# Performance work log

Measured on AMD Instinct MI355X. Metric: run time of the kernel, lower is better.

## Reference

```python
import jax, jax.numpy as jnp
from jax import lax
import numpy as np


def setup_inputs() -> dict:
    key = jax.random.key(0)
    ks = iter(jax.random.split(key, 48))

    def w(shape):
        fan = shape[0] if len(shape) == 2 else int(np.prod(shape[1:]))
        return jax.random.normal(next(ks), shape, jnp.float32) / np.sqrt(fan)

    def b(n):
        return jax.random.normal(next(ks), (n,), jnp.float32) * 0.01

    T = 16
    return dict(
        search=jax.random.normal(next(ks), (3, 383, 287), jnp.float32),
        exemplars=jax.random.normal(next(ks), (T, 3, 383, 287), jnp.float32),
        # AlexNet features (random-weight stand-in for pretrained)
        aw1=w((64, 3, 11, 11)), ab1=b(64),
        aw2=w((192, 64, 5, 5)), ab2=b(192),
        aw3=w((384, 192, 3, 3)), ab3=b(384),
        aw4=w((256, 384, 3, 3)), ab4=b(256),
        aw5=w((256, 256, 3, 3)), ab5=b(256),
        # conv_deconv: Conv1d(256,256,3,p=1) -> MaxPool1d(88) -> ConvTranspose1d(256,256,88)
        wcd=w((256, 256, 3)), bcd=b(256),
        wt=w((256, 256, 88)), bt=b(256),
        # st_gcn: GCN(256, 512, 256)
        ws1=w((256, 512)), bs1=b(512),
        ws2=w((512, 256)), bs2=b(256),
        # g, h: 1x1 Conv1d(256,256) == linear maps
        wg=w((256, 256)), bg=b(256),
        wh=w((256, 256)), bh=b(256),
        # ct_gcn: GCN(256, 384, 256)
        wc1=w((256, 384)), bc1=b(384),
        wc2=w((384, 256)), bc2=b(256),
    )


def _gct_forward(search, exemplars, aw1, ab1, aw2, ab2, aw3, ab3, aw4, ab4,
                 aw5, ab5, wcd, bcd, wt, bt, ws1, bs1, ws2, bs2,
                 wg, bg, wh, bh, wc1, bc1, wc2, bc2):
    f32 = jnp.float32

    def conv2d(x, w, bias, s, p):
        y = lax.conv_general_dilated(x, w, (s, s), [(p, p), (p, p)],
                                     dimension_numbers=('NCHW', 'OIHW', 'NCHW'))
        return y + bias[None, :, None, None]

    def maxpool(x):  # k=3, s=2, VALID (AlexNet pools)
        return lax.reduce_window(x, -jnp.inf, lax.max, (1, 1, 3, 3), (1, 1, 2, 2), 'VALID')

    def features(x):
        x = maxpool(jax.nn.relu(conv2d(x, aw1, ab1, 4, 2)))
        x = maxpool(jax.nn.relu(conv2d(x, aw2, ab2, 1, 2)))
        x = jax.nn.relu(conv2d(x, aw3, ab3, 1, 1))
        x = jax.nn.relu(conv2d(x, aw4, ab4, 1, 1))
        x = maxpool(jax.nn.relu(conv2d(x, aw5, ab5, 1, 1)))
        return x

    lrelu = lambda v: jax.nn.leaky_relu(v, 0.01)

    X = features(search[None])          # [1,256,11,8]
    Z = features(exemplars)             # [T,256,11,8]
    T = Z.shape[0]
    D = X.shape[1]                      # 256
    M = X.shape[2] * X.shape[3]         # 88
    Xf = X.reshape(D, M)                # [256,88]
    Zf = Z.reshape(T, D, M)             # [T,256,88]

    # conv_deconv branch: conv1d(k=3,p=1) -> global maxpool -> conv_transpose(k=M)
    xc = lax.conv_general_dilated(Xf[None], wcd, (1,), [(1, 1)],
                                  dimension_numbers=('NCH', 'OIH', 'NCH'))[0] + bcd[:, None]
    v = jnp.max(xc, axis=1)                              # [256]
    X_hat = jnp.einsum('i,iok->ok', v, wt) + bt[:, None]  # [256,88]

    # spatiotemporal graph: A[i+T*j, i+T*k]=1 for j!=k; self-loops for t!=0
    TM = T * M
    n = jnp.arange(TM)
    same_t = (n[:, None] % T) == (n[None, :] % T)
    diff_s = (n[:, None] // T) != (n[None, :] // T)
    A1 = (same_t & diff_s).astype(f32) + jnp.diag((n % T != 0).astype(f32))

    # st GCN over TM nodes (node n = t + T*m -> spatial-major flatten)
    nodes = Zf.transpose(2, 0, 1).reshape(TM, D)          # [TM,256]
    h1 = lrelu(A1 @ (nodes @ ws1) + bs1)                  # [TM,512]
    h2 = lrelu(A1 @ (h1 @ ws2) + bs2)                     # [TM,256]
    V1 = jnp.max(h2.reshape(M, T, D), axis=1).T           # temporal max-pool -> [256,88]

    # dynamic cross-track graph: pairwise g/h affinities + row softmax (fused)
    Vx = V1 + X_hat                                       # [256,88]
    G = wg @ Vx + bg[:, None]                             # [256,88]
    Hh = wh @ Vx + bh[:, None]                            # [256,88]
    A2 = jax.nn.softmax(Hh.T @ G, axis=1)                 # [88,88], A2[j,i]=g(i).h(j)

    # ct GCN
    xv = V1.T                                             # [88,256]
    c1 = lrelu(A2 @ (xv @ wc1) + bc1)                     # [88,384]
    V2 = lrelu(A2 @ (c1 @ wc2) + bc2).T                   # [256,88]

    # F.conv2d(X[1,256,11,8], V2[1,256,11,8]) -> full-overlap correlation = scalar
    R = jnp.sum(Xf * V2).reshape(1, 1, 1, 1)
    return R


def reference(search, exemplars, aw1, ab1, aw2, ab2, aw3, ab3, aw4, ab4,
              aw5, ab5, wcd, bcd, wt, bt, ws1, bs1, ws2, bs2,
              wg, bg, wh, bh, wc1, bc1, wc2, bc2):
    return _gct_forward(search, exemplars, aw1, ab1, aw2, ab2, aw3, ab3, aw4, ab4,
                        aw5, ab5, wcd, bcd, wt, bt, ws1, bs1, ws2, bs2,
                        wg, bg, wh, bh, wc1, bc1, wc2, bc2)
```

## Files before the change

### kernel.cpp

```cpp
#include <hip/hip_runtime.h>
#include <hip/hip_bf16.h>
#include <math.h>

#define BATCH 17
#define T_EX 16
#define H0 383
#define W0 287
#define C1 64
#define H1 95
#define W1 71
#define H1P 47
#define W1P 35
#define C2 192
#define H2P 23
#define W2P 17
#define C3 384
#define C45 256
#define H5P 11
#define W5P 8
#define DD 256
#define MM 88
#define TM 1408

#define HP1 389
#define WP1 292

typedef unsigned short ushort_t;
typedef __attribute__((ext_vector_type(8))) short short8;
typedef __attribute__((ext_vector_type(4))) float f32x4;

__device__ __forceinline__ float lrelu(float v) { return v > 0.f ? v : 0.01f * v; }

__device__ __forceinline__ ushort_t f2bf(float f) {
    unsigned int u = __float_as_uint(f);
    unsigned int r = (u + 0x7fffu + ((u >> 16) & 1u)) >> 16;
    return (ushort_t)r;
}
__device__ __forceinline__ float b2f(ushort_t b) {
    return __uint_as_float(((unsigned int)b) << 16);
}
__device__ __forceinline__ short8 ld16(const ushort_t* p) { return *(const short8*)p; }
__device__ __forceinline__ short8 ld2x8(const ushort_t* p) {
    union { uint2 u[2]; short8 s; } uu;
    uu.u[0] = *(const uint2*)p;
    uu.u[1] = *(const uint2*)(p + 4);
    return uu.s;
}
__device__ __forceinline__ void async_cp16(ushort_t* l, const ushort_t* g) {
    __builtin_amdgcn_global_load_lds(
        (const __attribute__((address_space(1))) void*)g,
        (__attribute__((address_space(3))) void*)l, 16, 0, 0);
}

__global__ void zfill_k(float4* __restrict__ p, int n4) {
    int idx = blockIdx.x * 256 + threadIdx.x;
    if (idx < n4) p[idx] = (float4){0.f, 0.f, 0.f, 0.f};
}

__global__ void prep1_k(const float* __restrict__ search, const float* __restrict__ exemp,
                        ushort_t* __restrict__ out) {
    int idx = blockIdx.x * 256 + threadIdx.x;
    if (idx >= BATCH * H0 * W0) return;
    int ix = idx % W0; int t = idx / W0;
    int iy = t % H0; int b = t / H0;
    const float* src = (b == 0) ? search : exemp + (size_t)(b - 1) * 3 * H0 * W0;
    const int hw = H0 * W0;
    float v0 = src[iy * W0 + ix];
    float v1 = src[hw + iy * W0 + ix];
    float v2 = src[2 * hw + iy * W0 + ix];
    ushort4 o;
    o.x = f2bf(v0); o.y = f2bf(v1); o.z = f2bf(v2); o.w = 0;
    *(ushort4*)&out[(((size_t)b * HP1 + iy + 2) * WP1 + ix + 2) * 4] = o;
}

__global__ void wprep_k(const float* __restrict__ w, ushort_t* __restrict__ out,
                        int KH, int KWl, int KWr, int CINl, int CINr,
                        int NKS, int nch) {
    int idx = blockIdx.x * 256 + threadIdx.x;
    if (idx >= nch) return;
    int c = idx & 255;
    int rest = idx >> 8;
    int ks = rest % NKS;
    int ocb = rest / NKS;
    int k8 = c >> 6, m = c & 63;
    int oc = ocb * 64 + m;
    int KWC = KWl * CINl;
    ushort_t* o = out + (size_t)idx * 8;
#pragma unroll
    for (int j = 0; j < 8; ++j) {
        int kg = ks * 32 + k8 * 8 + j;
        int ky = kg / KWC; int rem = kg - ky * KWC;
        int kx = rem / CINl; int ic = rem - kx * CINl;
        float v = 0.f;
        if (ky < KH && kx < KWr && ic < CINr)
            v = w[(((size_t)oc * CINr + ic) * KH + ky) * KWr + kx];
        o[j] = f2bf(v);
    }
}

__global__ void wprep_gemm_k(const float* __restrict__ ws1, const float* __restrict__ ws2,
                             const float* __restrict__ wcd, ushort_t* __restrict__ WS1T,
                             ushort_t* __restrict__ WS2T, ushort_t* __restrict__ WCDT) {
    int idx = blockIdx.x * 256 + threadIdx.x;
    const float* src; ushort_t* dst; int NKS, mode = 0, sa = 1, sk = 0, base;
    if (idx < 16384)       { src = ws1; dst = WS1T; NKS = 8;  sk = 512; base = idx; }
    else if (idx < 32768)  { src = ws2; dst = WS2T; NKS = 16; sk = 256; base = idx - 16384; }
    else if (idx < 57344)  { src = wcd; dst = WCDT; NKS = 24; mode = 1; base = idx - 32768; }
    else return;
    int c = base & 255;
    int rest = base >> 8;
    int ks = rest % NKS;
    int ocb = rest / NKS;
    int k8 = c >> 6, m = c & 63;
    int oc = ocb * 64 + m;
    ushort_t* o = dst + (size_t)base * 8;
#pragma unroll
    for (int j = 0; j < 8; ++j) {
        int kg = ks * 32 + k8 * 8 + j;
        float v;
        if (mode == 0) v = src[(size_t)oc * sa + (size_t)kg * sk];
        else           v = src[(size_t)oc * 768 + (kg & 255) * 3 + (kg >> 8)];
        o[j] = f2bf(v);
    }
}

template <int STRIDE, bool A16>
__global__ __launch_bounds__(256) void conv_mfma5(
    const ushort_t* __restrict__ inp, const ushort_t* __restrict__ wt,
    const float* __restrict__ bias, ushort_t* __restrict__ out,
    int Hp, int Wp, int C, int Wout, int HW, int NKS2, int KWl,
    int OHp, int OWp, int OPAD, int COUT) {
    const int tid = threadIdx.x;
    const int wv = tid >> 6, lane = tid & 63;
    const int quad = lane >> 4, l16 = lane & 15;
    const int n_blk = blockIdx.x * 64;
    const int ocb = blockIdx.y;
    const int b = blockIdx.z;

    __shared__ ushort_t As[2][4096];
    __shared__ ushort_t Bs[2][4096];
    __shared__ int offs[432];

    const int KWC = KWl * C;
    for (int g = tid; g < NKS2 * 8; g += 256) {
        int kg = g * 8;
        int ky = kg / KWC; int rem = kg - ky * KWC;
        int kx = rem / C; int c8 = rem - kx * C;
        offs[g] = (ky * Wp + kx) * C + c8;
    }

    const ushort_t* inb = inp + (size_t)b * Hp * Wp * C;
    int n_g = n_blk + lane;
    int n_gc = n_g < HW ? n_g : HW - 1;
    int oy = n_gc / Wout, ox = n_gc - oy * Wout;
    const int base0 = (oy * STRIDE * Wp + ox * STRIDE) * C;

    f32x4 acc[4];
#pragma unroll
    for (int cn = 0; cn < 4; ++cn) acc[cn] = (f32x4){0.f, 0.f, 0.f, 0.f};

    const ushort_t* wblk = wt + (size_t)ocb * (size_t)NKS2 * 4096;

    __syncthreads();

    {
        const ushort_t* aS = wblk + tid * 8;
        async_cp16(&As[0][tid * 8], aS);
        async_cp16(&As[0][2048 + tid * 8], aS + 2048);
        const int o0 = offs[wv], o1 = offs[4 + wv];
        if (A16) {
            async_cp16(&Bs[0][tid * 8], inb + base0 + o0);
            async_cp16(&Bs[0][2048 + tid * 8], inb + base0 + o1);
        } else {
            *(short8*)&Bs[0][tid * 8] = ld2x8(inb + base0 + o0);
            *(short8*)&Bs[0][2048 + tid * 8] = ld2x8(inb + base0 + o1);
        }
    }
    __syncthreads();

    for (int ks2 = 0; ks2 < NKS2; ++ks2) {
        const int cur = ks2 & 1, nxt = cur ^ 1;
        if (ks2 + 1 < NKS2) {
            const ushort_t* aS = wblk + (size_t)(ks2 + 1) * 4096 + tid * 8;
            async_cp16(&As[nxt][tid * 8], aS);
            async_cp16(&As[nxt][2048 + tid * 8], aS + 2048);
            const int o0 = offs[(ks2 + 1) * 8 + wv], o1 = offs[(ks2 + 1) * 8 + 4 + wv];
            if (A16) {
                async_cp16(&Bs[nxt][tid * 8], inb + base0 + o0);
                async_cp16(&Bs[nxt][2048 + tid * 8], inb + base0 + o1);
            } else {
                *(short8*)&Bs[nxt][tid * 8] = ld2x8(inb + base0 + o0);
                *(short8*)&Bs[nxt][2048 + tid * 8] = ld2x8(inb + base0 + o1);
            }
        }
#pragma unroll
        for (int h = 0; h < 2; ++h) {
            const short8 af = *(const short8*)&As[cur][h * 2048 + (quad * 64 + wv * 16 + l16) * 8];
#pragma unroll
            for (int cn = 0; cn < 4; ++cn) {
                const short8 bfr = *(const short8*)&Bs[cur][h * 2048 + (quad * 64 + cn * 16 + l16) * 8];
                acc[cn] = __builtin_amdgcn_mfma_f32_16x16x32_bf16(af, bfr, acc[cn], 0, 0, 0);
            }
        }
        __syncthreads();
    }

    const int oc0 = ocb * 64 + wv * 16 + quad * 4;
    const float bi0 = bias[oc0], bi1 = bias[oc0 + 1], bi2 = bias[oc0 + 2], bi3 = bias[oc0 + 3];
#pragma unroll
    for (int cn = 0; cn < 4; ++cn) {
        int n = n_blk + cn * 16 + l16;
        if (n < HW) {
            int y = n / Wout, x = n - y * Wout;
            size_t base = (((size_t)b * OHp + y + OPAD) * OWp + x + OPAD) * COUT + oc0;
            ushort4 o;
            o.x = f2bf(fmaxf(acc[cn][0] + bi0, 0.f));
            o.y = f2bf(fmaxf(acc[cn][1] + bi1, 0.f));
            o.z = f2bf(fmaxf(acc[cn][2] + bi2, 0.f));
            o.w = f2bf(fmaxf(acc[cn][3] + bi3, 0.f));
            *(ushort4*)&out[base] = o;
        }
    }
}

template <int MODE, bool HASBIAS, bool SC1>
__global__ __launch_bounds__(256) void gemm_mfma3(
    const ushort_t* __restrict__ Bsrc, const ushort_t* __restrict__ wt,
    const float* __restrict__ bias, float* __restrict__ out,
    int RS, int N, int NKS, int sn, int sc) {
    const int tid = threadIdx.x;
    const int wv = tid >> 6, lane = tid & 63;
    const int quad = lane >> 4, l16 = lane & 15;
    const int n_blk = blockIdx.x * 64;
    const int ocb = blockIdx.y;

    __shared__ ushort_t Bs[2][2048];

    int n_g = n_blk + lane;
    int n_gc = n_g < N ? n_g : N - 1;
    int row = (MODE == 1) ? (1 + (n_gc & 15)) * MM + (n_gc >> 4) : n_gc;
    const size_t base0 = (size_t)row * RS;

    f32x4 acc[4];
#pragma unroll
    for (int cn = 0; cn < 4; ++cn) acc[cn] = (f32x4){0.f, 0.f, 0.f, 0.f};

    const ushort_t* wblk = wt + (size_t)ocb * NKS * 2048;
    const int afrag = (quad * 64 + wv * 16 + l16) * 8;

    short8 a0 = ld16(wblk + afrag);
    *(short8*)&Bs[0][tid * 8] = ld16(Bsrc + base0 + wv * 8);
    __syncthreads();

    for (int ks = 0; ks < NKS; ++ks) {
        const int cur = ks & 1, nxt = cur ^ 1;
        short8 a1, bn;
        const bool more = (ks + 1 < NKS);
        if (more) {
            a1 = ld16(wblk + (ks + 1) * 2048 + afrag);
            bn = ld16(Bsrc + base0 + (ks + 1) * 32 + wv * 8);
        }
#pragma unroll
        for (int cn = 0; cn < 4; ++cn) {
            const short8 bfr = *(const short8*)&Bs[cur][(quad * 64 + cn * 16 + l16) * 8];
            acc[cn] = __builtin_amdgcn_mfma_f32_16x16x32_bf16(a0, bfr, acc[cn], 0, 0, 0);
        }
        if (more) *(short8*)&Bs[nxt][tid * 8] = bn;
        a0 = a1;
        __syncthreads();
    }

    const int oc0 = ocb * 64 + wv * 16 + quad * 4;
    float bb[4] = {0.f, 0.f, 0.f, 0.f};
    if (HASBIAS) { bb[0] = bias[oc0]; bb[1] = bias[oc0+1]; bb[2] = bias[oc0+2]; bb[3] = bias[oc0+3]; }
#pragma unroll
    for (int cn = 0; cn < 4; ++cn) {
        int n = n_blk + cn * 16 + l16;
        if (n < N) {
            if (SC1) {
                float4 o;
                o.x = acc[cn][0] + bb[0]; o.y = acc[cn][1] + bb[1];
                o.z = acc[cn][2] + bb[2]; o.w = acc[cn][3] + bb[3];
                *(float4*)&out[(size_t)n * sn + oc0] = o;
            } else {
#pragma unroll
                for (int reg = 0; reg < 4; ++reg)
                    out[(size_t)n * sn + (size_t)(oc0 + reg) * sc] = acc[cn][reg] + bb[reg];
            }
        }
    }
}

__global__ void pool_nhwc(const ushort_t* __restrict__ in, ushort_t* __restrict__ out,
                          int C, int Hin, int Win, int Hout, int Wout,
                          int OHp, int OWp, int OPAD) {
    int total = BATCH * C * Hout * Wout;
    int idx = blockIdx.x * 256 + threadIdx.x;
    if (idx >= total) return;
    int c = idx % C; int r = idx / C;
    int x = r % Wout; r /= Wout;
    int y = r % Hout; int b = r / Hout;
    const int rs = Win * C;
    const ushort_t* p = in + (((size_t)b * Hin + 2 * y) * Win + 2 * x) * C + c;
    float m = b2f(p[0]);
    m = fmaxf(m, b2f(p[C])); m = fmaxf(m, b2f(p[2 * C]));
    m = fmaxf(m, b2f(p[rs])); m = fmaxf(m, b2f(p[rs + C])); m = fmaxf(m, b2f(p[rs + 2 * C]));
    m = fmaxf(m, b2f(p[2 * rs])); m = fmaxf(m, b2f(p[2 * rs + C])); m = fmaxf(m, b2f(p[2 * rs + 2 * C]));
    out[(((size_t)b * OHp + y + OPAD) * OWp + x + OPAD) * C + c] = f2bf(m);
}

__global__ void pool5_k(const ushort_t* __restrict__ in, float* __restrict__ P,
                        ushort_t* __restrict__ PB, ushort_t* __restrict__ XfPad) {
    int total = BATCH * 256 * MM;
    int idx = blockIdx.x * 256 + threadIdx.x;
    if (idx >= total) return;
    int c = idx % 256; int r = idx / 256;
    int x = r % W5P; r /= W5P;
    int y = r % H5P; int b = r / H5P;
    const int rs = W2P * 256;
    const ushort_t* p = in + (((size_t)b * H2P + 2 * y) * W2P + 2 * x) * 256 + c;
    float m = b2f(p[0]);
    m = fmaxf(m, b2f(p[256])); m = fmaxf(m, b2f(p[512]));
    m = fmaxf(m, b2f(p[rs])); m = fmaxf(m, b2f(p[rs + 256])); m = fmaxf(m, b2f(p[rs + 512]));
    m = fmaxf(m, b2f(p[2 * rs])); m = fmaxf(m, b2f(p[2 * rs + 256])); m = fmaxf(m, b2f(p[2 * rs + 512]));
    int mm = y * W5P + x;
    size_t o = ((size_t)b * MM + mm) * 256 + c;
    P[o] = m;
    ushort_t mb = f2bf(m);
    PB[o] = mb;
    if (b == 0) XfPad[(size_t)(mm + 1) * 256 + c] = mb;
}

__global__ void vmax_k(const float* __restrict__ xc, float* __restrict__ v) {
    int c = blockIdx.x * 64 + threadIdx.x;
    float m = -INFINITY;
    for (int j = 0; j < MM; ++j) m = fmaxf(m, xc[(size_t)c * MM + j]);
    v[c] = m;
}

__global__ void xhat_k(const float* __restrict__ v, const float* __restrict__ wt,
                       const float* __restrict__ bt, float* __restrict__ xhat) {
    __shared__ float lv[256];
    for (int j = threadIdx.x; j < 256; j += 256) lv[j] = v[j];
    __syncthreads();
    int idx = blockIdx.x * 256 + threadIdx.x;
    if (idx >= DD * MM) return;
    int k = idx % MM, o = idx / MM;
    float acc = bt[o];
    for (int i = 0; i < 256; ++i) acc = fmaf(lv[i], wt[(i * 256 + o) * MM + k], acc);
    xhat[idx] = acc;
}

__global__ void s1_k(const float* __restrict__ Y1, float* __restrict__ S1) {
    int idx = blockIdx.x * 256 + threadIdx.x;
    if (idx >= T_EX * 512) return;
    int c = idx % 512, t = idx / 512;
    float acc = 0.f;
    for (int m = 0; m < MM; ++m) acc += Y1[(m * T_EX + t) * 512 + c];
    S1[idx] = acc;
}

__global__ void h1_k(const float* __restrict__ Y1, const float* __restrict__ S1,
                     const float* __restrict__ bs1, ushort_t* __restrict__ h1b) {
    int idx = blockIdx.x * 256 + threadIdx.x;
    if (idx >= TM * 512) return;
    int c = idx % 512; int n = idx / 512;
    int t = n % T_EX;
    float val = S1[t * 512 + c] + bs1[c];
    if (t == 0) val -= Y1[idx];
    h1b[idx] = f2bf(lrelu(val));
}

__global__ void s2_k(const float* __restrict__ Y2, float* __restrict__ S2) {
    int idx = blockIdx.x * 256 + threadIdx.x;
    if (idx >= T_EX * 256) return;
    int c = idx % 256, t = idx / 256;
    float acc = 0.f;
    for (int m = 0; m < MM; ++m) acc += Y2[(m * T_EX + t) * 256 + c];
    S2[idx] = acc;
}

__global__ void h2_k(const float* __restrict__ Y2, const float* __restrict__ S2,
                     const float* __restrict__ bs2, float* __restrict__ h2) {
    int idx = blockIdx.x * 256 + threadIdx.x;
    if (idx >= TM * 256) return;
    int c = idx % 256; int n = idx / 256;
    int t = n % T_EX;
    float val = S2[t * 256 + c] + bs2[c];
    if (t == 0) val -= Y2[idx];
    h2[idx] = lrelu(val);
}

__global__ void v1vx_k(const float* __restrict__ h2, const float* __restrict__ xhat,
                       float* __restrict__ V1, float* __restrict__ Vx) {
    int idx = blockIdx.x * 256 + threadIdx.x;
    if (idx >= DD * MM) return;
    int m = idx % MM, d = idx / MM;
    float mx = -INFINITY;
    for (int t = 0; t < T_EX; ++t) mx = fmaxf(mx, h2[(m * T_EX + t) * 256 + d]);
    V1[idx] = mx;
    Vx[idx] = mx + xhat[idx];
}

__global__ void lin88_k(const float* __restrict__ Wg, const float* __restrict__ bg,
                        const float* __restrict__ Wh, const float* __restrict__ bh,
                        const float* __restrict__ Vin, float* __restrict__ Gout,
                        float* __restrict__ Hout) {
    int idx = blockIdx.x * 256 + threadIdx.x;
    if (idx >= DD * MM) return;
    const float* W = blockIdx.y ? Wh : Wg;
    const float* bias = blockIdx.y ? bh : bg;
    float* out = blockIdx.y ? Hout : Gout;
    int m = idx % MM, o = idx / MM;
    const float* wr = W + o * 256;
    float acc = bias[o];
    for (int i = 0; i < 256; ++i) acc = fmaf(wr[i], Vin[i * MM + m], acc);
    out[idx] = acc;
}

__global__ void smsm_k(const float* __restrict__ Hh, const float* __restrict__ G,
                       float* __restrict__ A2) {
    int j = blockIdx.x;
    int tid = threadIdx.x;
    __shared__ float row[96];
    __shared__ float red[128];
    for (int i = tid; i < MM; i += 128) {
        float acc = 0.f;
        for (int c = 0; c < 256; ++c) acc = fmaf(Hh[c * MM + j], G[c * MM + i], acc);
        row[i] = acc;
    }
    __syncthreads();
    float val = (tid < MM) ? row[tid] : -INFINITY;
    red[tid] = val; __syncthreads();
    for (int s = 64; s > 0; s >>= 1) {
        if (tid < s) red[tid] = fmaxf(red[tid], red[tid + s]);
        __syncthreads();
    }
    float mx = red[0]; __syncthreads();
    float e = (tid < MM) ? expf(val - mx) : 0.f;
    red[tid] = e; __syncthreads();
    for (int s = 64; s > 0; s >>= 1) {
        if (tid < s) red[tid] += red[tid + s];
        __syncthreads();
    }
    float inv = 1.f / red[0];
    if (tid < MM) A2[j * MM + tid] = e * inv;
}

__global__ void t1_k(const float* __restrict__ V1, const float* __restrict__ wc1,
                     float* __restrict__ t1) {
    int idx = blockIdx.x * 256 + threadIdx.x;
    if (idx >= MM * 384) return;
    int c = idx % 384, m = idx / 384;
    float acc = 0.f;
    for (int d = 0; d < 256; ++d) acc = fmaf(V1[d * MM + m], wc1[d * 384 + c], acc);
    t1[idx] = acc;
}

__global__ void c1_k(const float* __restrict__ A2, const float* __restrict__ t1,
                     const float* __restrict__ bc1, float* __restrict__ c1) {
    int idx = blockIdx.x * 256 + threadIdx.x;
    if (idx >= MM * 384) return;
    int c = idx % 384, j = idx / 384;
    float acc = bc1[c];
    for (int i = 0; i < MM; ++i) acc = fmaf(A2[j * MM + i], t1[i * 384 + c], acc);
    c1[idx] = lrelu(acc);
}

__global__ void t2_k(const float* __restrict__ c1, const float* __restrict__ wc2,
                     float* __restrict__ t2) {
    int idx = blockIdx.x * 256 + threadIdx.x;
    if (idx >= MM * 256) return;
    int c = idx % 256, m = idx / 256;
    const float* cr = c1 + m * 384;
    float acc = 0.f;
    for (int d = 0; d < 384; ++d) acc = fmaf(cr[d], wc2[d * 256 + c], acc);
    t2[idx] = acc;
}

__global__ void v2_k(const float* __restrict__ A2, const float* __restrict__ t2,
                     const float* __restrict__ bc2, float* __restrict__ V2m) {
    int idx = blockIdx.x * 256 + threadIdx.x;
    if (idx >= MM * 256) return;
    int c = idx % 256, j = idx / 256;
    float acc = bc2[c];
    for (int i = 0; i < MM; ++i) acc = fmaf(A2[j * MM + i], t2[i * 256 + c], acc);
    V2m[idx] = lrelu(acc);
}

__global__ void final_k(const float* __restrict__ Xf2, const float* __restrict__ V2m,
                        float* __restrict__ out) {
    __shared__ float red[256];
    float acc = 0.f;
    for (int idx = threadIdx.x; idx < DD * MM; idx += 256)
        acc = fmaf(Xf2[idx], V2m[idx], acc);
    red[threadIdx.x] = acc; __syncthreads();
    for (int s = 128; s > 0; s >>= 1) {
        if (threadIdx.x < s) red[threadIdx.x] += red[threadIdx.x + s];
        __syncthreads();
    }
    if (threadIdx.x == 0) out[0] = red[0];
}

extern "C" void kernel_launch(void* const* d_in, const int* in_sizes, int n_in,
                              void* d_out, int out_size, void* d_ws, size_t ws_size,
                              hipStream_t stream) {
    const float* search = (const float*)d_in[0];
    const float* exemp  = (const float*)d_in[1];
    const float* aw1 = (const float*)d_in[2];  const float* ab1 = (const float*)d_in[3];
    const float* aw2 = (const float*)d_in[4];  const float* ab2 = (const float*)d_in[5];
    const float* aw3 = (const float*)d_in[6];  const float* ab3 = (const float*)d_in[7];
    const float* aw4 = (const float*)d_in[8];  const float* ab4 = (const float*)d_in[9];
    const float* aw5 = (const float*)d_in[10]; const float* ab5 = (const float*)d_in[11];
    const float* wcd = (const float*)d_in[12]; const float* bcd = (const float*)d_in[13];
    const float* wt  = (const float*)d_in[14]; const float* bt  = (const float*)d_in[15];
    const float* ws1 = (const float*)d_in[16]; const float* bs1 = (const float*)d_in[17];
    const float* ws2 = (const float*)d_in[18]; const float* bs2 = (const float*)d_in[19];
    const float* wg  = (const float*)d_in[20]; const float* bg  = (const float*)d_in[21];
    const float* wh  = (const float*)d_in[22]; const float* bh  = (const float*)d_in[23];
    const float* wc1 = (const float*)d_in[24]; const float* bc1 = (const float*)d_in[25];
    const float* wc2 = (const float*)d_in[26]; const float* bc2 = (const float*)d_in[27];

    float* ws = (float*)d_ws;
    float* R1 = ws;
    float* R2 = ws + 3870720;
    float* R3 = ws + 7544832;
    float* Wg = ws + 8628864;

    ushort_t* in1p  = (ushort_t*)R1;
    ushort_t* c1out = (ushort_t*)R2;
    ushort_t* p1out = (ushort_t*)R3;
    ushort_t* c2out = (ushort_t*)R1;
    ushort_t* p2out = (ushort_t*)R2;
    ushort_t* c3out = (ushort_t*)(R2 + 775200);
    ushort_t* c4out = (ushort_t*)R1;
    ushort_t* c5out = (ushort_t*)R3;
    ushort_t* WT    = (ushort_t*)Wg;

    zfill_k<<<(965500 + 255) / 256, 256, 0, stream>>>((float4*)R1, 965500);
    prep1_k<<<(BATCH * H0 * W0 + 255) / 256, 256, 0, stream>>>(search, exemp, in1p);
    wprep_k<<<(4608 + 255) / 256, 256, 0, stream>>>(aw1, WT, 11, 12, 11, 4, 3, 18, 4608);
    conv_mfma5<4, false><<<dim3(106, 1, BATCH), 256, 0, stream>>>(
        in1p, WT, ab1, c1out, HP1, WP1, 4, W1, H1 * W1, 9, 12, H1, W1, 0, 64);
    zfill_k<<<(270504 + 255) / 256, 256, 0, stream>>>((float4*)R3, 270504);
    pool_nhwc<<<(BATCH * 64 * H1P * W1P + 255) / 256, 256, 0, stream>>>(
        c1out, p1out, 64, H1, W1, H1P, W1P, 51, 39, 2);
    wprep_k<<<(38400 + 255) / 256, 256, 0, stream>>>(aw2, WT, 5, 5, 5, 64, 64, 50, 38400);
    conv_mfma5<1, true><<<dim3(26, 3, BATCH), 256, 0, stream>>>(
        p1out, WT, ab2, c2out, 51, 39, 64, W1P, H1P * W1P, 25, 5, H1P, W1P, 0, 192);
    zfill_k<<<(581400 + 255) / 256, 256, 0, stream>>>((float4*)R2, 581400);
    pool_nhwc<<<(BATCH * 192 * H2P * W2P + 255) / 256, 256, 0, stream>>>(
        c2out, p2out, 192, H1P, W1P, H2P, W2P, 25, 19, 1);
    wprep_k<<<(82944 + 255) / 256, 256, 0, stream>>>(aw3, WT, 3, 3, 3, 192, 192, 54, 82944);
    conv_mfma5<1, true><<<dim3(7, 6, BATCH), 256, 0, stream>>>(
        p2out, WT, ab3, c3out, 25, 19, 192, W2P, H2P * W2P, 27, 3, 25, 19, 1, 384);
    zfill_k<<<(258400 + 255) / 256, 256, 0, stream>>>((float4*)R1, 258400);
    wprep_k<<<(110592 + 255) / 256, 256, 0, stream>>>(aw4, WT, 3, 3, 3, 384, 384, 108, 110592);
    conv_mfma5<1, true><<<dim3(7, 4, BATCH), 256, 0, stream>>>(
        c3out, WT, ab4, c4out, 25, 19, 384, W2P, H2P * W2P, 54, 3, 25, 19, 1, 256);
    wprep_k<<<(73728 + 255) / 256, 256, 0, stream>>>(aw5, WT, 3, 3, 3, 256, 256, 72, 73728);
    conv_mfma5<1, true><<<dim3(7, 4, BATCH), 256, 0, stream>>>(
        c4out, WT, ab5, c5out, 25, 19, 256, W2P, H2P * W2P, 36, 3, H2P, W2P, 0, 256);

    float*    P      = R1 + 2417664;
    ushort_t* PB     = (ushort_t*)(R1 + 2800640);
    ushort_t* XfPad  = (ushort_t*)(R1 + 2992128);
    float*    xc     = R1 + 3003648;

    ushort_t* WS1T = (ushort_t*)Wg;
    ushort_t* WS2T = (ushort_t*)(Wg + 65536);
    ushort_t* WCDT = (ushort_t*)(Wg + 131072);
    wprep_gemm_k<<<(57344 + 255) / 256, 256, 0, stream>>>(ws1, ws2, wcd, WS1T, WS2T, WCDT);

    pool5_k<<<(BATCH * 256 * MM + 255) / 256, 256, 0, stream>>>(c5out, P, PB, XfPad);
    float* Xf2 = P;

    float* v_   = R1 + 0;
    float* xhat = R1 + 1024;
    float* Y1   = R1 + 23552;
    float* S1   = R1 + 744448;
    ushort_t* h1b = (ushort_t*)(R1 + 752640);
    float* Y2   = R1 + 1473536;
    float* S2   = R1 + 1833984;
    float* h2   = R1 + 1838080;
    float* V1   = R1 + 2198528;
    float* Vx   = R1 + 2221056;
    float* G    = R1 + 2243584;
    float* Hh   = R1 + 2266112;
    float* A2   = R1 + 2296832;
    float* t1   = R1 + 2305024;
    float* c1   = R1 + 2338816;
    float* t2   = R1 + 2372608;
    float* V2m  = R1 + 2395136;

    gemm_mfma3<0, true, false><<<dim3(2, 4), 256, 0, stream>>>(
        XfPad, WCDT, bcd, xc, 256, MM, 24, 1, MM);
    vmax_k<<<4, 64, 0, stream>>>(xc, v_);
    xhat_k<<<(DD * MM + 255) / 256, 256, 0, stream>>>(v_, wt, bt, xhat);

    gemm_mfma3<1, false, true><<<dim3(22, 8), 256, 0, stream>>>(
        PB, WS1T, nullptr, Y1, 256, TM, 8, 512, 1);
    s1_k<<<(T_EX * 512 + 255) / 256, 256, 0, stream>>>(Y1, S1);
    h1_k<<<(TM * 512 + 255) / 256, 256, 0, stream>>>(Y1, S1, bs1, h1b);
    gemm_mfma3<0, false, true><<<dim3(22, 4), 256, 0, stream>>>(
        h1b, WS2T, nullptr, Y2, 512, TM, 16, 256, 1);
    s2_k<<<(T_EX * 256 + 255) / 256, 256, 0, stream>>>(Y2, S2);
    h2_k<<<(TM * 256 + 255) / 256, 256, 0, stream>>>(Y2, S2, bs2, h2);
    v1vx_k<<<(DD * MM + 255) / 256, 256, 0, stream>>>(h2, xhat, V1, Vx);

    lin88_k<<<dim3((DD * MM + 255) / 256, 2), 256, 0, stream>>>(wg, bg, wh, bh, Vx, G, Hh);
    smsm_k<<<MM, 128, 0, stream>>>(Hh, G, A2);

    t1_k<<<(MM * 384 + 255) / 256, 256, 0, stream>>>(V1, wc1, t1);
    c1_k<<<(MM * 384 + 255) / 256, 256, 0, stream>>>(A2, t1, bc1, c1);
    t2_k<<<(MM * 256 + 255) / 256, 256, 0, stream>>>(c1, wc2, t2);
    v2_k<<<(MM * 256 + 255) / 256, 256, 0, stream>>>(A2, t2, bc2, V2m);

    final_k<<<1, 256, 0, stream>>>(Xf2, V2m, (float*)d_out);
}
```

Baseline: 547.6 us.

## Register-stage conv B tiles with XOR-swizzled LDS and fuse small epilogue kernels

The conv kernel's B-operand (activation) loads for the A16 path now go through registers and are written into a swizzled LDS layout after the MFMA loop, instead of direct async copies. Each 8-lane group fetches one pixel's contiguous channels, and the XOR swizzle is meant to reduce LDS bank conflicts on the fragment reads. Separately, the vmax+xhat kernels and the s1/h1 and s2/h2 reduction/broadcast pairs are each fused into a single kernel to cut launches and intermediate buffers. wprep_k also gains an output-channel bound guard. The register staging trades async overlap for coalescing and conflict-free reads, and the fused kernels run far fewer threads per pass.

```diff
diff --git a/kernel.cpp b/kernel.cpp
--- a/kernel.cpp
+++ b/kernel.cpp
@@ -75,7 +75,7 @@
 
 __global__ void wprep_k(const float* __restrict__ w, ushort_t* __restrict__ out,
                         int KH, int KWl, int KWr, int CINl, int CINr,
-                        int NKS, int nch) {
+                        int NKS, int nch, int OCr) {
     int idx = blockIdx.x * 256 + threadIdx.x;
     if (idx >= nch) return;
     int c = idx & 255;
@@ -92,7 +92,7 @@
         int ky = kg / KWC; int rem = kg - ky * KWC;
         int kx = rem / CINl; int ic = rem - kx * CINl;
         float v = 0.f;
-        if (ky < KH && kx < KWr && ic < CINr)
+        if (oc < OCr && ky < KH && kx < KWr && ic < CINr)
             v = w[(((size_t)oc * CINr + ic) * KH + ky) * KWr + kx];
         o[j] = f2bf(v);
     }
@@ -125,7 +125,7 @@
 }
 
 template <int STRIDE, bool A16>
-__global__ __launch_bounds__(256) void conv_mfma5(
+__global__ __launch_bounds__(256) void conv_mfma13(
     const ushort_t* __restrict__ inp, const ushort_t* __restrict__ wt,
     const float* __restrict__ bias, ushort_t* __restrict__ out,
     int Hp, int Wp, int C, int Wout, int HW, int NKS2, int KWl,
@@ -150,10 +150,25 @@
     }
 
     const ushort_t* inb = inp + (size_t)b * Hp * Wp * C;
+
+    const int g8 = lane & 7, po = lane >> 3;
+    int np0 = n_blk + wv * 16 + po;      if (np0 >= HW) np0 = HW - 1;
+    int np1 = n_blk + wv * 16 + 8 + po;  if (np1 >= HW) np1 = HW - 1;
+    const ushort_t* bsrc0;
+    const ushort_t* bsrc1;
+    {
+        int oy0 = np0 / Wout, ox0 = np0 - oy0 * Wout;
+        int oy1 = np1 / Wout, ox1 = np1 - oy1 * Wout;
+        bsrc0 = inb + (size_t)(oy0 * STRIDE * Wp + ox0 * STRIDE) * C;
+        bsrc1 = inb + (size_t)(oy1 * STRIDE * Wp + ox1 * STRIDE) * C;
+    }
+    const int ws0 = g8 * 512 + (((wv * 16 + po) ^ g8) * 8);
+    const int ws1 = g8 * 512 + (((wv * 16 + 8 + po) ^ g8) * 8);
+
     int n_g = n_blk + lane;
     int n_gc = n_g < HW ? n_g : HW - 1;
-    int oy = n_gc / Wout, ox = n_gc - oy * Wout;
-    const int base0 = (oy * STRIDE * Wp + ox * STRIDE) * C;
+    int oyl = n_gc / Wout, oxl = n_gc - oyl * Wout;
+    const int base0 = (oyl * STRIDE * Wp + oxl * STRIDE) * C;
 
     f32x4 acc[4];
 #pragma unroll
@@ -167,11 +182,13 @@
         const ushort_t* aS = wblk + tid * 8;
         async_cp16(&As[0][tid * 8], aS);
         async_cp16(&As[0][2048 + tid * 8], aS + 2048);
-        const int o0 = offs[wv], o1 = offs[4 + wv];
-        if (A16) {
-            async_cp16(&Bs[0][tid * 8], inb + base0 + o0);
-            async_cp16(&Bs[0][2048 + tid * 8], inb + base0 + o1);
+        if constexpr (A16) {
+            short8 r0v = ld16(bsrc0 + offs[g8]);
+            short8 r1v = ld16(bsrc1 + offs[g8]);
+            *(short8*)&Bs[0][ws0] = r0v;
+            *(short8*)&Bs[0][ws1] = r1v;
         } else {
+            const int o0 = offs[wv], o1 = offs[4 + wv];
             *(short8*)&Bs[0][tid * 8] = ld2x8(inb + base0 + o0);
             *(short8*)&Bs[0][2048 + tid * 8] = ld2x8(inb + base0 + o1);
         }
@@ -180,15 +197,17 @@
 
     for (int ks2 = 0; ks2 < NKS2; ++ks2) {
         const int cur = ks2 & 1, nxt = cur ^ 1;
-        if (ks2 + 1 < NKS2) {
+        const bool more = (ks2 + 1 < NKS2);
+        short8 rb0, rb1;
+        if (more) {
             const ushort_t* aS = wblk + (size_t)(ks2 + 1) * 4096 + tid * 8;
             async_cp16(&As[nxt][tid * 8], aS);
             async_cp16(&As[nxt][2048 + tid * 8], aS + 2048);
-            const int o0 = offs[(ks2 + 1) * 8 + wv], o1 = offs[(ks2 + 1) * 8 + 4 + wv];
-            if (A16) {
-                async_cp16(&Bs[nxt][tid * 8], inb + base0 + o0);
-                async_cp16(&Bs[nxt][2048 + tid * 8], inb + base0 + o1);
+            if constexpr (A16) {
+                rb0 = ld16(bsrc0 + offs[(ks2 + 1) * 8 + g8]);
+                rb1 = ld16(bsrc1 + offs[(ks2 + 1) * 8 + g8]);
             } else {
+                const int o0 = offs[(ks2 + 1) * 8 + wv], o1 = offs[(ks2 + 1) * 8 + 4 + wv];
                 *(short8*)&Bs[nxt][tid * 8] = ld2x8(inb + base0 + o0);
                 *(short8*)&Bs[nxt][2048 + tid * 8] = ld2x8(inb + base0 + o1);
             }
@@ -198,8 +217,19 @@
             const short8 af = *(const short8*)&As[cur][h * 2048 + (quad * 64 + wv * 16 + l16) * 8];
 #pragma unroll
             for (int cn = 0; cn < 4; ++cn) {
-                const short8 bfr = *(const short8*)&Bs[cur][h * 2048 + (quad * 64 + cn * 16 + l16) * 8];
+                int bidx;
+                if constexpr (A16)
+                    bidx = h * 2048 + quad * 512 + (((cn * 16 + l16) ^ (h * 4 + quad)) * 8);
+                else
+                    bidx = h * 2048 + (quad * 64 + cn * 16 + l16) * 8;
+                const short8 bfr = *(const short8*)&Bs[cur][bidx];
                 acc[cn] = __builtin_amdgcn_mfma_f32_16x16x32_bf16(af, bfr, acc[cn], 0, 0, 0);
+            }
+        }
+        if constexpr (A16) {
+            if (more) {
+                *(short8*)&Bs[nxt][ws0] = rb0;
+                *(short8*)&Bs[nxt][ws1] = rb1;
             }
         }
         __syncthreads();
@@ -331,17 +361,16 @@
     if (b == 0) XfPad[(size_t)(mm + 1) * 256 + c] = mb;
 }
 
-__global__ void vmax_k(const float* __restrict__ xc, float* __restrict__ v) {
-    int c = blockIdx.x * 64 + threadIdx.x;
-    float m = -INFINITY;
-    for (int j = 0; j < MM; ++j) m = fmaxf(m, xc[(size_t)c * MM + j]);
-    v[c] = m;
-}
-
-__global__ void xhat_k(const float* __restrict__ v, const float* __restrict__ wt,
-                       const float* __restrict__ bt, float* __restrict__ xhat) {
+__global__ void xhat2_k(const float* __restrict__ xc, const float* __restrict__ wt,
+                        const float* __restrict__ bt, float* __restrict__ xhat) {
     __shared__ float lv[256];
-    for (int j = threadIdx.x; j < 256; j += 256) lv[j] = v[j];
+    {
+        int j = threadIdx.x;
+        const float* xr = xc + (size_t)j * MM;
+        float mx = xr[0];
+        for (int k = 1; k < MM; ++k) mx = fmaxf(mx, xr[k]);
+        lv[j] = mx;
+    }
     __syncthreads();
     int idx = blockIdx.x * 256 + threadIdx.x;
     if (idx >= DD * MM) return;
@@ -351,44 +380,41 @@
     xhat[idx] = acc;
 }
 
-__global__ void s1_k(const float* __restrict__ Y1, float* __restrict__ S1) {
+__global__ void sh1_k(const float* __restrict__ Y1, const float* __restrict__ bs1,
+                      ushort_t* __restrict__ h1b) {
     int idx = blockIdx.x * 256 + threadIdx.x;
     if (idx >= T_EX * 512) return;
-    int c = idx % 512, t = idx / 512;
-    float acc = 0.f;
-    for (int m = 0; m < MM; ++m) acc += Y1[(m * T_EX + t) * 512 + c];
-    S1[idx] = acc;
-}
-
-__global__ void h1_k(const float* __restrict__ Y1, const float* __restrict__ S1,
-                     const float* __restrict__ bs1, ushort_t* __restrict__ h1b) {
-    int idx = blockIdx.x * 256 + threadIdx.x;
-    if (idx >= TM * 512) return;
-    int c = idx % 512; int n = idx / 512;
-    int t = n % T_EX;
-    float val = S1[t * 512 + c] + bs1[c];
-    if (t == 0) val -= Y1[idx];
-    h1b[idx] = f2bf(lrelu(val));
-}
-
-__global__ void s2_k(const float* __restrict__ Y2, float* __restrict__ S2) {
+    int c = idx & 511, t = idx >> 9;
+    float s = 0.f;
+    for (int m = 0; m < MM; ++m) s += Y1[(size_t)(m * T_EX + t) * 512 + c];
+    float base = s + bs1[c];
+    if (t == 0) {
+        for (int m = 0; m < MM; ++m) {
+            float val = base - Y1[(size_t)(m * T_EX) * 512 + c];
+            h1b[(size_t)(m * T_EX) * 512 + c] = f2bf(lrelu(val));
+        }
+    } else {
+        ushort_t v = f2bf(lrelu(base));
+        for (int m = 0; m < MM; ++m)
+            h1b[(size_t)(m * T_EX + t) * 512 + c] = v;
+    }
+}
+
+__global__ void sh2_k(const float* __restrict__ Y2, const float* __restrict__ bs2,
+                      float* __restrict__ h2) {
     int idx = blockIdx.x * 256 + threadIdx.x;
     if (idx >= T_EX * 256) return;
-    int c = idx % 256, t = idx / 256;
-    float acc = 0.f;
-    for (int m = 0; m < MM; ++m) acc += Y2[(m * T_EX + t) * 256 + c];
-    S2[idx] = acc;
-}
-
-__global__ void h2_k(const float* __restrict__ Y2, const float* __restrict__ S2,
-                     const float* __restrict__ bs2, float* __restrict__ h2) {
-    int idx = blockIdx.x * 256 + threadIdx.x;
-    if (idx >= TM * 256) return;
-    int c = idx % 256; int n = idx / 256;
-    int t = n % T_EX;
-    float val = S2[t * 256 + c] + bs2[c];
-    if (t == 0) val -= Y2[idx];
-    h2[idx] = lrelu(val);
+    int c = idx & 255, t = idx >> 8;
+    float s = 0.f;
+    for (int m = 0; m < MM; ++m) s += Y2[(size_t)(m * T_EX + t) * 256 + c];
+    float base = s + bs2[c];
+    if (t == 0) {
+        for (int m = 0; m < MM; ++m)
+            h2[(size_t)(m * T_EX) * 256 + c] = lrelu(base - Y2[(size_t)(m * T_EX) * 256 + c]);
+    } else {
+        float v = lrelu(base);
+        for (int m = 0; m < MM; ++m) h2[(size_t)(m * T_EX + t) * 256 + c] = v;
+    }
 }
 
 __global__ void v1vx_k(const float* __restrict__ h2, const float* __restrict__ xhat,
@@ -539,27 +565,27 @@
 
     zfill_k<<<(965500 + 255) / 256, 256, 0, stream>>>((float4*)R1, 965500);
     prep1_k<<<(BATCH * H0 * W0 + 255) / 256, 256, 0, stream>>>(search, exemp, in1p);
-    wprep_k<<<(4608 + 255) / 256, 256, 0, stream>>>(aw1, WT, 11, 12, 11, 4, 3, 18, 4608);
-    conv_mfma5<4, false><<<dim3(106, 1, BATCH), 256, 0, stream>>>(
+    wprep_k<<<(4608 + 255) / 256, 256, 0, stream>>>(aw1, WT, 11, 12, 11, 4, 3, 18, 4608, 64);
+    conv_mfma13<4, false><<<dim3(106, 1, BATCH), 256, 0, stream>>>(
         in1p, WT, ab1, c1out, HP1, WP1, 4, W1, H1 * W1, 9, 12, H1, W1, 0, 64);
     zfill_k<<<(270504 + 255) / 256, 256, 0, stream>>>((float4*)R3, 270504);
     pool_nhwc<<<(BATCH * 64 * H1P * W1P + 255) / 256, 256, 0, stream>>>(
         c1out, p1out, 64, H1, W1, H1P, W1P, 51, 39, 2);
-    wprep_k<<<(38400 + 255) / 256, 256, 0, stream>>>(aw2, WT, 5, 5, 5, 64, 64, 50, 38400);
-    conv_mfma5<1, true><<<dim3(26, 3, BATCH), 256, 0, stream>>>(
+    wprep_k<<<(38400 + 255) / 256, 256, 0, stream>>>(aw2, WT, 5, 5, 5, 64, 64, 50, 38400, 192);
+    conv_mfma13<1, true><<<dim3(26, 3, BATCH), 256, 0, stream>>>(
         p1out, WT, ab2, c2out, 51, 39, 64, W1P, H1P * W1P, 25, 5, H1P, W1P, 0, 192);
     zfill_k<<<(581400 + 255) / 256, 256, 0, stream>>>((float4*)R2, 581400);
     pool_nhwc<<<(BATCH * 192 * H2P * W2P + 255) / 256, 256, 0, stream>>>(
         c2out, p2out, 192, H1P, W1P, H2P, W2P, 25, 19, 1);
-    wprep_k<<<(82944 + 255) / 256, 256, 0, stream>>>(aw3, WT, 3, 3, 3, 192, 192, 54, 82944);
-    conv_mfma5<1, true><<<dim3(7, 6, BATCH), 256, 0, stream>>>(
+    wprep_k<<<(82944 + 255) / 256, 256, 0, stream>>>(aw3, WT, 3, 3, 3, 192, 192, 54, 82944, 384);
+    conv_mfma13<1, true><<<dim3(7, 6, BATCH), 256, 0, stream>>>(
         p2out, WT, ab3, c3out, 25, 19, 192, W2P, H2P * W2P, 27, 3, 25, 19, 1, 384);
     zfill_k<<<(258400 + 255) / 256, 256, 0, stream>>>((float4*)R1, 258400);
-    wprep_k<<<(110592 + 255) / 256, 256, 0, stream>>>(aw4, WT, 3, 3, 3, 384, 384, 108, 110592);
-    conv_mfma5<1, true><<<dim3(7, 4, BATCH), 256, 0, stream>>>(
+    wprep_k<<<(110592 + 255) / 256, 256, 0, stream>>>(aw4, WT, 3, 3, 3, 384, 384, 108, 110592, 256);
+    conv_mfma13<1, true><<<dim3(7, 4, BATCH), 256, 0, stream>>>(
         c3out, WT, ab4, c4out, 25, 19, 384, W2P, H2P * W2P, 54, 3, 25, 19, 1, 256);
-    wprep_k<<<(73728 + 255) / 256, 256, 0, stream>>>(aw5, WT, 3, 3, 3, 256, 256, 72, 73728);
-    conv_mfma5<1, true><<<dim3(7, 4, BATCH), 256, 0, stream>>>(
+    wprep_k<<<(73728 + 255) / 256, 256, 0, stream>>>(aw5, WT, 3, 3, 3, 256, 256, 72, 73728, 256);
+    conv_mfma13<1, true><<<dim3(7, 4, BATCH), 256, 0, stream>>>(
         c4out, WT, ab5, c5out, 25, 19, 256, W2P, H2P * W2P, 36, 3, H2P, W2P, 0, 256);
 
     float*    P      = R1 + 2417664;
@@ -575,13 +601,10 @@
     pool5_k<<<(BATCH * 256 * MM + 255) / 256, 256, 0, stream>>>(c5out, P, PB, XfPad);
     float* Xf2 = P;
 
-    float* v_   = R1 + 0;
     float* xhat = R1 + 1024;
     float* Y1   = R1 + 23552;
-    float* S1   = R1 + 744448;
     ushort_t* h1b = (ushort_t*)(R1 + 752640);
     float* Y2   = R1 + 1473536;
-    float* S2   = R1 + 1833984;
     float* h2   = R1 + 1838080;
     float* V1   = R1 + 2198528;
     float* Vx   = R1 + 2221056;
@@ -595,17 +618,14 @@
 
     gemm_mfma3<0, true, false><<<dim3(2, 4), 256, 0, stream>>>(
         XfPad, WCDT, bcd, xc, 256, MM, 24, 1, MM);
-    vmax_k<<<4, 64, 0, stream>>>(xc, v_);
-    xhat_k<<<(DD * MM + 255) / 256, 256, 0, stream>>>(v_, wt, bt, xhat);
+    xhat2_k<<<(DD * MM + 255) / 256, 256, 0, stream>>>(xc, wt, bt, xhat);
 
     gemm_mfma3<1, false, true><<<dim3(22, 8), 256, 0, stream>>>(
         PB, WS1T, nullptr, Y1, 256, TM, 8, 512, 1);
-    s1_k<<<(T_EX * 512 + 255) / 256, 256, 0, stream>>>(Y1, S1);
-    h1_k<<<(TM * 512 + 255) / 256, 256, 0, stream>>>(Y1, S1, bs1, h1b);
+    sh1_k<<<(T_EX * 512 + 255) / 256, 256, 0, stream>>>(Y1, bs1, h1b);
     gemm_mfma3<0, false, true><<<dim3(22, 4), 256, 0, stream>>>(
         h1b, WS2T, nullptr, Y2, 512, TM, 16, 256, 1);
-    s2_k<<<(T_EX * 256 + 255) / 256, 256, 0, stream>>>(Y2, S2);
-    h2_k<<<(TM * 256 + 255) / 256, 256, 0, stream>>>(Y2, S2, bs2, h2);
+    sh2_k<<<(T_EX * 256 + 255) / 256, 256, 0, stream>>>(Y2, bs2, h2);
     v1vx_k<<<(DD * MM + 255) / 256, 256, 0, stream>>>(h2, xhat, V1, Vx);
 
     lin88_k<<<dim3((DD * MM + 255) / 256, 2), 256, 0, stream>>>(wg, bg, wh, bh, Vx, G, Hh);
```

Result: no change. 548.2 us (+0.1%).
